# Performance work log

Hardware: AMD Instinct MI355X
Metric: run time of the kernel (lower is better)

Reference implementation:

```python
import jax, jax.numpy as jnp
import numpy as np

K_PERIODS = 6


def setup_inputs() -> dict:
    key = jax.random.key(0)
    x = jax.random.normal(key, (16, 2048, 128), dtype=jnp.float32)
    return {"x": x}


def reference(x):
    # x: [B, T, N] -> out: [B, K, Pmax, N].
    # Pmax is data-dependent in the torch original (max selected period); here we
    # use the static upper bound Pmax = T so shapes are jit-static. Columns
    # p >= P_row are zero, matching the original's zero padding.
    B, T, N = x.shape
    BN = B * N
    seqs = jnp.transpose(x, (0, 2, 1)).reshape(BN, T)  # [BN, T]

    # --- top-k nonzero frequencies by spectral energy ---
    spec = jnp.fft.rfft(seqs, axis=-1)
    mag2 = spec.real ** 2 + spec.imag ** 2
    mag2 = mag2.at[:, 0].set(0.0)  # kill DC bin
    k = min(K_PERIODS, mag2.shape[-1] - 1)
    _, kidx = jax.lax.top_k(mag2, k)          # [BN, K]
    kidx = jnp.maximum(kidx, 1)

    # --- per-(row, freq) period geometry ---
    P = jnp.maximum(T // kidx, 1)             # [BN, K] period length
    cycles = jnp.maximum(T // P, 1)           # [BN, K] number of full cycles
    take = cycles * P
    base = jnp.maximum(T - take, 0)           # [BN, K] start offset

    # --- fold-and-average via scatter-add (no [BN,K,Cmax,Pmax] blowup) ---
    # element at time t >= base maps to phase p = (t - base) % P, averaged over cycles
    t = jnp.arange(T, dtype=jnp.int32)
    rel = t[None, None, :] - base[:, :, None]          # [BN, K, T]
    valid = rel >= 0
    p = jnp.where(valid, rel % P[:, :, None], 0)       # phase index in [0, P)
    vals = jnp.where(valid, seqs[:, None, :], 0.0)     # [BN, K, T]

    row = jnp.arange(BN * k, dtype=jnp.int32).reshape(BN, k, 1)
    seg_ids = row * T + p                               # flat segment id
    sums = jax.ops.segment_sum(vals.reshape(-1), seg_ids.reshape(-1),
                               num_segments=BN * k * T)
    seg = sums.reshape(BN, k, T) / cycles[:, :, None].astype(vals.dtype)

    out = seg.reshape(B, N, k, T).transpose(0, 2, 3, 1)  # [B, K, Pmax=T, N]
    return out
```

## Files before the change

kernel.cpp:

```cpp
#include <hip/hip_runtime.h>
#include <stdint.h>

#define TB   256
#define TLEN 2048
#define NB   16
#define NCH  128
#define BN   (NB*NCH)
#define KP   6

typedef unsigned long long u64;

__device__ inline float2 cmul(float2 a, float2 b) {
  return make_float2(a.x * b.x - a.y * b.y, a.x * b.y + a.y * b.x);
}
__device__ inline float2 cadd(float2 a, float2 b) { return make_float2(a.x + b.x, a.y + b.y); }
__device__ inline float2 csub(float2 a, float2 b) { return make_float2(a.x - b.x, a.y - b.y); }
__device__ inline float2 cmni(float2 a) { return make_float2(a.y, -a.x); }

#define PAD(o) ((o) + ((o) >> 4))
#define C2 0.70710678118654752f

__device__ inline void radix8(const float2 A[8], float2 w1, float2 B[8]) {
  float2 s02 = cadd(A[0], A[4]), d02 = csub(A[0], A[4]);
  float2 s13 = cadd(A[2], A[6]), d13 = csub(A[2], A[6]);
  float2 E0 = cadd(s02, s13), E1 = cadd(d02, cmni(d13));
  float2 E2 = csub(s02, s13), E3 = csub(d02, cmni(d13));
  float2 t02 = cadd(A[1], A[5]), e02 = csub(A[1], A[5]);
  float2 t13 = cadd(A[3], A[7]), e13 = csub(A[3], A[7]);
  float2 O0 = cadd(t02, t13), O1 = cadd(e02, cmni(e13));
  float2 O2 = csub(t02, t13), O3 = csub(e02, cmni(e13));
  float2 T0 = O0;
  float2 T1 = make_float2(C2 * (O1.x + O1.y), C2 * (O1.y - O1.x));
  float2 T2 = cmni(O2);
  float2 T3 = make_float2(C2 * (O3.y - O3.x), -C2 * (O3.x + O3.y));
  float2 b0 = cadd(E0, T0), b4 = csub(E0, T0);
  float2 b1 = cadd(E1, T1), b5 = csub(E1, T1);
  float2 b2 = cadd(E2, T2), b6 = csub(E2, T2);
  float2 b3 = cadd(E3, T3), b7 = csub(E3, T3);
  float2 w2 = cmul(w1, w1);
  float2 w3 = cmul(w2, w1);
  float2 w4 = cmul(w2, w2);
  float2 w5 = cmul(w4, w1);
  float2 w6 = cmul(w4, w2);
  float2 w7 = cmul(w4, w3);
  B[0] = b0;
  B[1] = cmul(w1, b1);
  B[2] = cmul(w2, b2);
  B[3] = cmul(w3, b3);
  B[4] = cmul(w4, b4);
  B[5] = cmul(w5, b5);
  B[6] = cmul(w6, b6);
  B[7] = cmul(w7, b7);
}

__global__ __launch_bounds__(256) void k_prep(const float* __restrict__ x,
                                              float* __restrict__ seqs,
                                              float4* __restrict__ out4, int n4) {
  int bid = blockIdx.x;
  if (bid < 1024) {
    __shared__ float tile[64][65];
    int tb = bid & 31, nb = (bid >> 5) & 1, b = bid >> 6;
    int t0 = tb * 64, n0 = nb * 64;
    int tx = threadIdx.x & 63, ty = threadIdx.x >> 6;
#pragma unroll
    for (int tt = ty; tt < 64; tt += 4)
      tile[tt][tx] = x[(size_t)(b * TLEN + t0 + tt) * NCH + n0 + tx];
    __syncthreads();
#pragma unroll
    for (int nn = ty; nn < 64; nn += 4)
      seqs[(size_t)(b * NCH + n0 + nn) * TLEN + t0 + tx] = tile[tx][nn];
  } else {
    int i = (bid - 1024) * 256 + threadIdx.x;
    if (i < n4) out4[i] = make_float4(0.f, 0.f, 0.f, 0.f);
  }
}

__global__ __launch_bounds__(256) void k_fft_fold(const float* __restrict__ seqs,
                                                  float* __restrict__ out) {
  __shared__ __align__(16) float2 bufA[2176];
  __shared__ __align__(16) float2 bufB[2176];
  __shared__ float2 tw[256];
  __shared__ int4 prm[2][KP];
  int tid = threadIdx.x, lane = tid & 63, wv = tid >> 6;
  int r0 = blockIdx.x * 2;
  const float* row0 = seqs + (size_t)r0 * TLEN;

#pragma unroll
  for (int kk = 0; kk < 8; kk++) {
    int t = tid + kk * TB;
    bufA[PAD(t)] = make_float2(row0[t], row0[t + TLEN]);
  }
  {
    float sn, cs;
    sincosf((-6.283185307179586f / 2048.f) * (float)tid, &sn, &cs);
    tw[tid & 255] = make_float2(cs, sn);
  }

#pragma unroll
  for (int stage = 0; stage < 3; stage++) {
    int s = (stage == 0) ? 1 : (stage == 1) ? 8 : 64;
    float2* xb = (stage == 1) ? bufB : bufA;
    float2* yb = (stage == 1) ? bufA : bufB;
    __syncthreads();
    int i = tid;
    int q = i & (s - 1);
    int cb = i - q;
    float2 A[8], B[8];
#pragma unroll
    for (int j = 0; j < 8; j++) A[j] = xb[PAD(i + j * 256)];
    radix8(A, tw[cb], B);
    int o = q + 8 * cb;
#pragma unroll
    for (int j = 0; j < 8; j++) yb[PAD(o + j * s)] = B[j];
  }
  __syncthreads();
#pragma unroll
  for (int ii = 0; ii < 2; ii++) {
    int i = tid + ii * TB;
    float2 a0 = bufB[PAD(i)], a1 = bufB[PAD(i + 512)];
    float2 a2 = bufB[PAD(i + 1024)], a3 = bufB[PAD(i + 1536)];
    float2 S02 = cadd(a0, a2), D02 = csub(a0, a2);
    float2 S13 = cadd(a1, a3), D13 = csub(a1, a3);
    bufA[PAD(i)]        = cadd(S02, S13);
    bufA[PAD(i + 512)]  = cadd(D02, cmni(D13));
    bufA[PAD(i + 1024)] = csub(S02, S13);
    bufA[PAD(i + 1536)] = csub(D02, cmni(D13));
  }
  __syncthreads();

  const float2* Z = bufA;
  float* srows = (float*)bufB;

  if (wv < 2) {
    u64 kr[16];
#pragma unroll
    for (int j = 0; j < 16; j++) {
      int kb = lane * 16 + j + 1;
      float2 zk = Z[PAD(kb)];
      float2 zc = Z[PAD(2048 - kb)];
      float m2;
      if (wv == 0) {
        float ax = zk.x + zc.x, ay = zk.y - zc.y;
        m2 = ax * ax + ay * ay;
      } else {
        float bx = zk.x - zc.x, by = zk.y + zc.y;
        m2 = bx * bx + by * by;
      }
      kr[j] = ((u64)__float_as_uint(m2) << 32) | (unsigned)(0xFFFFFFFFu - (unsigned)kb);
    }
#pragma unroll 1
    for (int r = 0; r < KP; r++) {
      u64 m = kr[0];
#pragma unroll
      for (int j = 1; j < 16; j++) m = kr[j] > m ? kr[j] : m;
#pragma unroll
      for (int off = 1; off < 64; off <<= 1) {
        u64 o = __shfl_xor(m, off);
        m = o > m ? o : m;
      }
#pragma unroll
      for (int j = 0; j < 16; j++)
        if (kr[j] == m) kr[j] = 0ull;
      if (lane == 0) {
        int bin = (int)(0xFFFFFFFFu - (unsigned)(m & 0xFFFFFFFFull));
        if (bin < 1 || bin > 1024) bin = 1;
        int P = TLEN / bin;
        int cyc = TLEN / P;
        int base = TLEN - cyc * P;
        prm[wv][r] = make_int4(P, base, cyc, 0);
      }
    }
  } else {
    const float4* s4 = (const float4*)row0;
    float4* r4 = (float4*)srows;
    for (int i = tid - 128; i < 1024; i += 128) r4[i] = s4[i];
  }
  __syncthreads();

  for (int task = wv; task < 2 * KP; task += 4) {
    int rw = task & 1, k = task >> 1;
    int4 pr = prm[rw][k];
    int P = pr.x, base = pr.y, cyc = pr.z;
    float inv = 1.0f / (float)cyc;
    const float* srow = srows + rw * TLEN;
    int row = r0 + rw, b = row >> 7, n = row & 127;
    float* dst = out + (size_t)(b * KP + k) * TLEN * NCH + n;

    if (P >= 64) {
      for (int p = lane; p < P; p += 64) {
        const float* sp = srow + base + p;
        float s = 0.f;
        for (int c = 0; c < cyc; c++) s += sp[c * P];
        dst[(size_t)p * NCH] = s * inv;
      }
    } else {
      int wc = 64 / P, u = wc * P, ci = lane / P;
      float v = 0.f;
      if (lane < u) {
        for (int c0 = 0; c0 < cyc; c0 += wc) {
          int c = c0 + ci;
          if (c < cyc) v += srow[base + c0 * P + lane];
        }
      }
      for (int s = P; s < u; s <<= 1) {
        float o = __shfl_down(v, s);
        if (lane + s < u) v += o;
      }
      if (lane < P) dst[(size_t)lane * NCH] = v * inv;
    }
  }
}

extern "C" void kernel_launch(void* const* d_in, const int* in_sizes, int n_in,
                              void* d_out, int out_size, void* d_ws, size_t ws_size,
                              hipStream_t stream) {
  const float* x = (const float*)d_in[0];
  float* out = (float*)d_out;
  float* seqs = (float*)d_ws;

  int n4 = out_size / 4;
  int fill_blocks = (n4 + 255) / 256;
  k_prep<<<1024 + fill_blocks, 256, 0, stream>>>(x, seqs, (float4*)out, n4);
  k_fft_fold<<<BN / 2, 256, 0, stream>>>(seqs, out);
}
```

Before: 144.2 us.

## Process four rows per block with two packed complex FFTs

Each block now handles four sequences, as two complex FFTs of packed real pairs, instead of two. The block count is halved. All four waves now do top-k selection, one per row, rather than two waves selecting while two copy. The aim is to spread the twiddle setup, the syncs and the per-block overhead over more work and to keep all waves busy. In exchange, shared memory per block roughly doubles (about 70KB), which lowers occupancy and may reduce latency hiding.

```diff
diff --git a/kernel.cpp b/kernel.cpp
--- a/kernel.cpp
+++ b/kernel.cpp
@@ -77,18 +77,23 @@
 
 __global__ __launch_bounds__(256) void k_fft_fold(const float* __restrict__ seqs,
                                                   float* __restrict__ out) {
-  __shared__ __align__(16) float2 bufA[2176];
-  __shared__ __align__(16) float2 bufB[2176];
+  __shared__ __align__(16) float2 bufA[2][2176];
+  __shared__ __align__(16) float2 bufB[2][2176];
   __shared__ float2 tw[256];
-  __shared__ int4 prm[2][KP];
+  __shared__ int4 prm[4][KP];
   int tid = threadIdx.x, lane = tid & 63, wv = tid >> 6;
-  int r0 = blockIdx.x * 2;
+  int r0 = blockIdx.x * 4;
+  int b = r0 >> 7, n0 = r0 & 127;
   const float* row0 = seqs + (size_t)r0 * TLEN;
 
 #pragma unroll
-  for (int kk = 0; kk < 8; kk++) {
-    int t = tid + kk * TB;
-    bufA[PAD(t)] = make_float2(row0[t], row0[t + TLEN]);
+  for (int pp = 0; pp < 2; pp++) {
+    const float* rp = row0 + pp * 2 * TLEN;
+#pragma unroll
+    for (int kk = 0; kk < 8; kk++) {
+      int t = tid + kk * TB;
+      bufA[pp][PAD(t)] = make_float2(rp[t], rp[t + TLEN]);
+    }
   }
   {
     float sn, cs;
@@ -99,39 +104,53 @@
 #pragma unroll
   for (int stage = 0; stage < 3; stage++) {
     int s = (stage == 0) ? 1 : (stage == 1) ? 8 : 64;
-    float2* xb = (stage == 1) ? bufB : bufA;
-    float2* yb = (stage == 1) ? bufA : bufB;
     __syncthreads();
     int i = tid;
     int q = i & (s - 1);
     int cb = i - q;
-    float2 A[8], B[8];
-#pragma unroll
-    for (int j = 0; j < 8; j++) A[j] = xb[PAD(i + j * 256)];
-    radix8(A, tw[cb], B);
+    float2 w1 = tw[cb];
     int o = q + 8 * cb;
 #pragma unroll
-    for (int j = 0; j < 8; j++) yb[PAD(o + j * s)] = B[j];
+    for (int pp = 0; pp < 2; pp++) {
+      float2* xb = (stage == 1) ? bufB[pp] : bufA[pp];
+      float2* yb = (stage == 1) ? bufA[pp] : bufB[pp];
+      float2 A[8], B[8];
+#pragma unroll
+      for (int j = 0; j < 8; j++) A[j] = xb[PAD(i + j * 256)];
+      radix8(A, w1, B);
+#pragma unroll
+      for (int j = 0; j < 8; j++) yb[PAD(o + j * s)] = B[j];
+    }
   }
   __syncthreads();
 #pragma unroll
-  for (int ii = 0; ii < 2; ii++) {
-    int i = tid + ii * TB;
-    float2 a0 = bufB[PAD(i)], a1 = bufB[PAD(i + 512)];
-    float2 a2 = bufB[PAD(i + 1024)], a3 = bufB[PAD(i + 1536)];
-    float2 S02 = cadd(a0, a2), D02 = csub(a0, a2);
-    float2 S13 = cadd(a1, a3), D13 = csub(a1, a3);
-    bufA[PAD(i)]        = cadd(S02, S13);
-    bufA[PAD(i + 512)]  = cadd(D02, cmni(D13));
-    bufA[PAD(i + 1024)] = csub(S02, S13);
-    bufA[PAD(i + 1536)] = csub(D02, cmni(D13));
+  for (int pp = 0; pp < 2; pp++) {
+#pragma unroll
+    for (int ii = 0; ii < 2; ii++) {
+      int i = tid + ii * TB;
+      float2 a0 = bufB[pp][PAD(i)], a1 = bufB[pp][PAD(i + 512)];
+      float2 a2 = bufB[pp][PAD(i + 1024)], a3 = bufB[pp][PAD(i + 1536)];
+      float2 S02 = cadd(a0, a2), D02 = csub(a0, a2);
+      float2 S13 = cadd(a1, a3), D13 = csub(a1, a3);
+      bufA[pp][PAD(i)]        = cadd(S02, S13);
+      bufA[pp][PAD(i + 512)]  = cadd(D02, cmni(D13));
+      bufA[pp][PAD(i + 1024)] = csub(S02, S13);
+      bufA[pp][PAD(i + 1536)] = csub(D02, cmni(D13));
+    }
   }
   __syncthreads();
 
-  const float2* Z = bufA;
-  float* srows = (float*)bufB;
-
-  if (wv < 2) {
+#pragma unroll
+  for (int pp = 0; pp < 2; pp++) {
+    const float4* s4 = (const float4*)(row0 + pp * 2 * TLEN);
+    float4* r4 = (float4*)bufB[pp];
+#pragma unroll
+    for (int ii = 0; ii < 4; ii++) r4[tid + ii * TB] = s4[tid + ii * TB];
+  }
+
+  {
+    const float2* Z = bufA[wv >> 1];
+    int hw = wv & 1;
     u64 kr[16];
 #pragma unroll
     for (int j = 0; j < 16; j++) {
@@ -139,7 +158,7 @@
       float2 zk = Z[PAD(kb)];
       float2 zc = Z[PAD(2048 - kb)];
       float m2;
-      if (wv == 0) {
+      if (hw == 0) {
         float ax = zk.x + zc.x, ay = zk.y - zc.y;
         m2 = ax * ax + ay * ay;
       } else {
@@ -170,20 +189,16 @@
         prm[wv][r] = make_int4(P, base, cyc, 0);
       }
     }
-  } else {
-    const float4* s4 = (const float4*)row0;
-    float4* r4 = (float4*)srows;
-    for (int i = tid - 128; i < 1024; i += 128) r4[i] = s4[i];
   }
   __syncthreads();
 
-  for (int task = wv; task < 2 * KP; task += 4) {
-    int rw = task & 1, k = task >> 1;
+  for (int task = wv; task < 4 * KP; task += 4) {
+    int rw = task & 3, k = task >> 2;
     int4 pr = prm[rw][k];
     int P = pr.x, base = pr.y, cyc = pr.z;
     float inv = 1.0f / (float)cyc;
-    const float* srow = srows + rw * TLEN;
-    int row = r0 + rw, b = row >> 7, n = row & 127;
+    const float* srow = (const float*)bufB[rw >> 1] + (rw & 1) * TLEN;
+    int n = n0 + rw;
     float* dst = out + (size_t)(b * KP + k) * TLEN * NCH + n;
 
     if (P >= 64) {
@@ -221,5 +236,5 @@
   int n4 = out_size / 4;
   int fill_blocks = (n4 + 255) / 256;
   k_prep<<<1024 + fill_blocks, 256, 0, stream>>>(x, seqs, (float4*)out, n4);
-  k_fft_fold<<<BN / 2, 256, 0, stream>>>(seqs, out);
-}
+  k_fft_fold<<<BN / 4, 256, 0, stream>>>(seqs, out);
+}
```

New measurement: 150.3 us. 1.04x slower.
